# Kernel optimization log

Measured on AMD Instinct MI355X. Metric: run time of the kernel, lower is better.

Reference implementation:

```python
import jax, jax.numpy as jnp
import numpy as np

DIM = 64; N_LAYER = 2; B = 2048; M = 64
N_ENT = 100000; N_REL = 200
TEMP = 0.2; KGE_W = 1e-6
MIN_N = 1e-15; BND = 1e-5


def _norm(x):
    return jnp.sqrt(jnp.clip((x * x).sum(-1, keepdims=True), MIN_N))


def _l2(x):
    # F.normalize(p=2): x / max(||x||, 1e-12)
    return x / jnp.maximum(jnp.sqrt((x * x).sum(-1, keepdims=True)), 1e-12)


def _artanh(x):
    return jnp.arctanh(jnp.clip(x, -1.0 + BND, 1.0 - BND))


def expmap0(u):
    n = _norm(u)
    return jnp.tanh(n) * u / n


def logmap0(x):
    n = _norm(x)
    return _artanh(n) * x / n


def mobius_add(x, y):
    x2 = (x * x).sum(-1, keepdims=True)
    y2 = (y * y).sum(-1, keepdims=True)
    xy = (x * y).sum(-1, keepdims=True)
    num = (1 + 2 * xy + y2) * x + (1 - x2) * y
    den = 1 + 2 * xy + x2 * y2
    return num / jnp.clip(den, MIN_N)


def expmap(u, p):
    lam = 2.0 / jnp.clip(1.0 - (p * p).sum(-1, keepdims=True), MIN_N)
    n = _norm(u)
    return mobius_add(p, jnp.tanh(lam * n / 2.0) * u / n)


def logmap(x, p):
    m = mobius_add(-p, x)
    n = _norm(m)
    lam = 2.0 / jnp.clip(1.0 - (p * p).sum(-1, keepdims=True), MIN_N)
    return (2.0 / lam) * _artanh(n) * m / n


def _ed_agg(h, path, t, att_w1, att_w2):
    # attention: Linear(2d,d,no bias) -> LeakyReLU(0)==ReLU -> Linear(d,1,no bias) -> Sigmoid
    x = jnp.concatenate([h, path], -1)                       # [B,M,2d]
    a = jax.nn.sigmoid(jax.nn.relu(x @ att_w1) @ att_w2)[..., 0]  # [B,M]
    w = jax.nn.softmax(a, axis=-1)
    return (w[..., None] * t).sum(1)                          # [B,d]


def _hyper_agg(h, path, t, curvature, a2_w1, a2_b1, a2_w2, a2_b2):
    h, path, t = _l2(h), _l2(path), _l2(t)
    hh = expmap0(h) * jnp.abs(curvature)
    ht = expmap(t, hh)
    hr = expmap(path, hh)
    tang = logmap0(jnp.concatenate([hh, hr], -1))            # [B,M,2d]
    a = jnp.tanh(jax.nn.relu(tang @ a2_w1 + a2_b1) @ a2_w2 + a2_b2)[..., 0]
    w = jax.nn.softmax(a, axis=-1)                            # [B,M]
    agg = w[..., None] * ht
    mean_pt = (w[..., None] * hh).sum(1, keepdims=True)       # [B,1,d]
    e = logmap(agg, mean_pt)
    return (w[..., None] * e).sum(1)                          # [B,d]


def _build(E, R, h_idx, r_idx, t_idx, init_emb, agg):
    embs = [init_emb]
    for i in range(N_LAYER):
        h = E[h_idx[0]]
        path = R[r_idx[0]]
        for k in range(1, i + 1):  # faithful to source: inner loop reuses index i
            h = h + E[h_idx[i]]
            path = path * R[r_idx[i]]
        embs.append(agg(h, path, E[t_idx[i]]))
    return jnp.stack(embs)  # [L+1, B, d]


def _mlcl(a_stack, b_stack):
    # vectorized over layer index i of MLCL_Loss(a[i], b[i], a_list, b_list)
    na, nb = _l2(a_stack), _l2(b_stack)                       # [L+1,B,d]
    d = na.shape[-1]
    pos = (na * nb).sum(-1)                                   # [L+1,B]
    ttl1 = jnp.einsum('lbd,md->lbm', na, nb.reshape(-1, d))
    ttl2 = jnp.einsum('lbd,md->lbm', nb, na.reshape(-1, d))
    ep = jnp.exp(pos / TEMP)
    l1 = -jnp.log(ep / jnp.exp(ttl1 / TEMP).sum(-1)).sum()
    l2 = -jnp.log(ep / jnp.exp(ttl2 / TEMP).sum(-1)).sum()
    return KGE_W * (l1 + l2)


def _cat_rev(stack):
    # e = stack[0]; for i in 1..L: e = cat(stack[i], e) -> [L, L-1, ..., 0]
    return jnp.concatenate([stack[i] for i in range(stack.shape[0] - 1, -1, -1)], -1)


def setup_inputs() -> dict:
    key = jax.random.key(0)
    ks = jax.random.split(key, 24)
    def ent_idx(k):
        return jax.random.randint(k, (N_LAYER, B, M), 0, N_ENT, dtype=jnp.int32)
    def rel_idx(k):
        return jax.random.randint(k, (N_LAYER, B, M), 0, N_REL, dtype=jnp.int32)
    inp = {
        'items': jax.random.randint(ks[0], (B,), 0, N_ENT, dtype=jnp.int32),
        'ucf_h': ent_idx(ks[1]), 'ucf_r': rel_idx(ks[2]), 'ucf_t': ent_idx(ks[3]),
        'ikg_h': ent_idx(ks[4]), 'ikg_r': rel_idx(ks[5]), 'ikg_t': ent_idx(ks[6]),
        'ukg_h': ent_idx(ks[7]), 'ukg_r': rel_idx(ks[8]), 'ukg_t': ent_idx(ks[9]),
        'icf_h': ent_idx(ks[10]), 'icf_r': rel_idx(ks[11]), 'icf_t': ent_idx(ks[12]),
        'ent_emb': jax.random.normal(ks[13], (N_ENT, DIM), jnp.float32) * 0.02,
        'rel_emb': jax.random.normal(ks[14], (N_REL, DIM), jnp.float32) * 0.02,
        'att_w1': jax.random.normal(ks[15], (2 * DIM, DIM), jnp.float32) * 0.05,
        'att_w2': jax.random.normal(ks[16], (DIM, 1), jnp.float32) * 0.05,
        'att2_w1': jax.random.normal(ks[17], (2 * DIM, DIM), jnp.float32) * 0.05,
        'att2_b1': jnp.zeros((DIM,), jnp.float32),
        'att2_w2': jax.random.normal(ks[18], (DIM, 1), jnp.float32) * 0.05,
        'att2_b2': jnp.zeros((1,), jnp.float32),
        'curvature': jnp.asarray(1.0, jnp.float32),
    }
    return inp


def reference(items, ucf_h, ucf_r, ucf_t, ikg_h, ikg_r, ikg_t,
              ukg_h, ukg_r, ukg_t, icf_h, icf_r, icf_t,
              ent_emb, rel_emb, att_w1, att_w2,
              att2_w1, att2_b1, att2_w2, att2_b2, curvature):
    ed = lambda h, p, t: _ed_agg(h, p, t, att_w1, att_w2)
    hy = lambda h, p, t: _hyper_agg(h, p, t, curvature, att2_w1, att2_b1, att2_w2, att2_b2)
    ucf = _build(ent_emb, rel_emb, ucf_h, ucf_r, ucf_t, ent_emb[ucf_h[0]].mean(1), ed)
    ikg = _build(ent_emb, rel_emb, ikg_h, ikg_r, ikg_t, ent_emb[items], ed)
    ukg = _build(ent_emb, rel_emb, ukg_h, ukg_r, ukg_t, ent_emb[ukg_h[0]].mean(1), hy)
    icf = _build(ent_emb, rel_emb, icf_h, icf_r, icf_t, ent_emb[icf_h[0]].mean(1), hy)
    kge_loss = _mlcl(ucf, ukg) + _mlcl(ikg, icf)
    e_u = jnp.concatenate([_cat_rev(ucf), _cat_rev(ukg)], -1)
    e_i = jnp.concatenate([_cat_rev(icf), _cat_rev(ikg)], -1)
    scores = jax.nn.sigmoid((e_i * e_u).sum(-1))
    return scores, kge_loss
```

## Files before the change

kernel.cpp:

```cpp
#include <hip/hip_runtime.h>
#include <hip/hip_bf16.h>
#include <cstdint>
#include <cstddef>

constexpr int NB = 2048;
constexpr int NM = 64;
constexpr int ND = 64;
constexpr int NBM = NB * NM;
constexpr int NROWS = 3 * NB;
constexpr int STACK = 3 * NB * ND;
constexpr int NZ = 8;

typedef __attribute__((ext_vector_type(8))) short short8;
typedef __attribute__((ext_vector_type(4))) float float4v;

__device__ __forceinline__ float wsum(float v) {
#pragma unroll
  for (int o = 32; o > 0; o >>= 1) v += __shfl_xor(v, o, 64);
  return v;
}

__device__ __forceinline__ float wmax(float v) {
#pragma unroll
  for (int o = 32; o > 0; o >>= 1) v = fmaxf(v, __shfl_xor(v, o, 64));
  return v;
}

__device__ __forceinline__ float rcpf(float x) { return __builtin_amdgcn_rcpf(x); }
__device__ __forceinline__ float sqf(float x) { return __builtin_amdgcn_sqrtf(x); }

__device__ __forceinline__ float fast_tanh(float x) {
  float t = __expf(2.f * x);
  return (t - 1.f) * rcpf(t + 1.f);
}

__device__ __forceinline__ float artanh_clip(float x) {
  x = fminf(fmaxf(x, -1.f + 1e-5f), 1.f - 1e-5f);
  return 0.5f * __logf((1.f + x) * rcpf(1.f - x));
}

__device__ __forceinline__ ushort f2bf(float f) {
  return (ushort)((__float_as_uint(f) + 0x8000u) >> 16);
}
__device__ __forceinline__ float bf2f(ushort u) {
  return __uint_as_float((uint)u << 16);
}
__device__ __forceinline__ uint pack_bf2(float h, float p) {
  uint hu = __float_as_uint(h) + 0x8000u;
  uint pu = __float_as_uint(p) + 0x8000u;
  return __builtin_amdgcn_perm(pu, hu, 0x07060302);
}
__device__ __forceinline__ float hp_lo(uint v) { return __uint_as_float(v << 16); }
__device__ __forceinline__ float hp_hi(uint v) { return __uint_as_float(v & 0xFFFF0000u); }

__device__ __forceinline__ float readlane_f(float v, int l) {
  return __int_as_float(__builtin_amdgcn_readlane(__float_as_int(v), l));
}

__device__ __forceinline__ void write_row_norm(
    float v, float* __restrict__ frow, ushort* __restrict__ nrow, int lane) {
  float nv = wsum(v * v);
  float r = rcpf(fmaxf(sqf(nv), 1e-12f));
  frow[lane] = v;
  nrow[lane] = f2bf(v * r);
}

__global__ __launch_bounds__(64) void prep_kernel(
    const float* __restrict__ E, const int* __restrict__ items,
    const float* __restrict__ w1_ed, const float* __restrict__ w1_hy,
    float* __restrict__ s_ikg, ushort* __restrict__ nbf_ikg,
    ushort* __restrict__ w1p_ed, ushort* __restrict__ w1p_hy) {
  int blk = blockIdx.x, lane = threadIdx.x;
  if (blk < NB) {
    float v = E[(size_t)items[blk] * ND + lane];
    write_row_norm(v, s_ikg + (size_t)blk * ND, nbf_ikg + (size_t)blk * ND, lane);
  } else {
    int e = (blk - NB) * 64 + lane;
    const float* w1 = (e < 8192) ? w1_ed : w1_hy;
    ushort* out = (e < 8192) ? w1p_ed : w1p_hy;
    e &= 8191;
    int j = e & 7, ln = (e >> 3) & 63, nt = (e >> 9) & 3, kt = e >> 11;
    int n = nt * 16 + (ln & 15), k = kt * 32 + ((ln >> 4) << 3) + j;
    out[e] = f2bf(w1[k * 64 + n]);
  }
}

constexpr int OFF_H = 0;
constexpr int OFF_P = 4608;
constexpr int OFF_T = 9728;
constexpr int XS = 152;
constexpr int REGA_SZ = 14336;

__global__ __launch_bounds__(256) void agg_all_kernel(
    const float* __restrict__ E, const float* __restrict__ R,
    const int* __restrict__ h0, const int* __restrict__ r0, const int* __restrict__ t0,
    const int* __restrict__ h1, const int* __restrict__ r1, const int* __restrict__ t1,
    const int* __restrict__ h2, const int* __restrict__ r2, const int* __restrict__ t2,
    const int* __restrict__ h3, const int* __restrict__ r3, const int* __restrict__ t3,
    const ushort* __restrict__ w1p_ed, const float* __restrict__ w2_ed,
    const ushort* __restrict__ w1p_hy, const float* __restrict__ b1,
    const float* __restrict__ w2_hy, const float* __restrict__ b2,
    const float* __restrict__ curv,
    float* __restrict__ stacks, ushort* __restrict__ nbf) {
  __shared__ __align__(16) ushort regA[REGA_SZ];
  __shared__ float a_s[64];
  __shared__ float part[4][64];
  __shared__ float minit[4][64];

  const int b = blockIdx.x;
  const int fam = blockIdx.y;
  const int tid = threadIdx.x;
  const int wave = tid >> 6, lane = tid & 63;
  const int m0 = __builtin_amdgcn_readfirstlane(wave) * 16;
  const int colq = lane & 15, quad = lane >> 4;
  const size_t L = (size_t)NB * ND;

  const int* h_idx = (fam == 0) ? h0 : (fam == 1) ? h1 : (fam == 2) ? h2 : h3;
  const int* r_idx = (fam == 0) ? r0 : (fam == 1) ? r1 : (fam == 2) ? r2 : r3;
  const int* t_idx = (fam == 0) ? t0 : (fam == 1) ? t1 : (fam == 2) ? t2 : t3;
  float* sb = stacks + (size_t)fam * STACK;
  ushort* nb = nbf + (size_t)fam * STACK;

  uint hp[16];

  if (fam < 2) {
    const int do_init = (fam == 0);
    for (int layer = 0; layer < 2; ++layer) {
      float tv[16];
      if (layer == 0) {
        float macc = 0.f;
#pragma unroll
        for (int mi = 0; mi < 16; ++mi) {
          const int m = m0 + mi;
          float hd = E[(size_t)h_idx[b * NM + m] * ND + lane];
          float pd = R[(size_t)r_idx[b * NM + m] * ND + lane];
          macc += hd;
          uint pk = pack_bf2(hd, pd);
          hp[mi] = pk;
          regA[m * XS + lane] = (ushort)pk;
          regA[m * XS + 64 + lane] = (ushort)(pk >> 16);
        }
        if (do_init) minit[wave][lane] = macc;
      } else {
#pragma unroll
        for (int mi = 0; mi < 16; ++mi) {
          const int m = m0 + mi;
          float hd = hp_lo(hp[mi]) + E[(size_t)h_idx[NBM + b * NM + m] * ND + lane];
          float pd = hp_hi(hp[mi]) * R[(size_t)r_idx[NBM + b * NM + m] * ND + lane];
          uint pk = pack_bf2(hd, pd);
          hp[mi] = pk;
          regA[m * XS + lane] = (ushort)pk;
          regA[m * XS + 64 + lane] = (ushort)(pk >> 16);
        }
      }
#pragma unroll
      for (int mi = 0; mi < 16; ++mi)
        tv[mi] = E[(size_t)t_idx[(size_t)layer * NBM + b * NM + m0 + mi] * ND + lane];

      {
        short8 afr[4];
#pragma unroll
        for (int kt = 0; kt < 4; ++kt)
          afr[kt] = *(const short8*)&regA[(m0 + colq) * XS + kt * 32 + quad * 8];
        float w2v[4];
#pragma unroll
        for (int nt = 0; nt < 4; ++nt) w2v[nt] = w2_ed[nt * 16 + colq];
        float cc[4][4];
#pragma unroll
        for (int nt = 0; nt < 4; ++nt) {
          float4v c = {0.f, 0.f, 0.f, 0.f};
#pragma unroll
          for (int kt = 0; kt < 4; ++kt) {
            short8 bfr = *(const short8*)&w1p_ed[(((kt << 2) | nt) * 64 + lane) * 8];
            c = __builtin_amdgcn_mfma_f32_16x16x32_bf16(afr[kt], bfr, c, 0, 0, 0);
          }
#pragma unroll
          for (int i = 0; i < 4; ++i) cc[nt][i] = c[i];
        }
        float sred[4];
#pragma unroll
        for (int i = 0; i < 4; ++i)
          sred[i] = fmaxf(cc[0][i], 0.f) * w2v[0] + fmaxf(cc[1][i], 0.f) * w2v[1] +
                    fmaxf(cc[2][i], 0.f) * w2v[2] + fmaxf(cc[3][i], 0.f) * w2v[3];
#pragma unroll
        for (int o = 8; o > 0; o >>= 1) {
#pragma unroll
          for (int i = 0; i < 4; ++i) sred[i] += __shfl_xor(sred[i], o, 64);
        }
        if (colq == 0) {
#pragma unroll
          for (int i = 0; i < 4; ++i)
            a_s[m0 + quad * 4 + i] = 1.f / (1.f + __expf(-sred[i]));
        }
      }
      __syncthreads();

      float wl;
      {
        float v = a_s[lane];
        float mx = wmax(v);
        float e = __expf(v - mx);
        wl = e / wsum(e);
      }
      if (layer == 0 && do_init && wave == 0) {
        float v = (minit[0][lane] + minit[1][lane] + minit[2][lane] + minit[3][lane]) * (1.f / 64.f);
        write_row_norm(v, sb + (size_t)b * ND, nb + (size_t)b * ND, lane);
      }

      float o = 0.f;
#pragma unroll
      for (int mi = 0; mi < 16; ++mi)
        o = fmaf(readlane_f(wl, m0 + mi), tv[mi], o);
      part[wave][lane] = o;
      __syncthreads();
      if (wave == 0) {
        float v = part[0][lane] + part[1][lane] + part[2][lane] + part[3][lane];
        write_row_norm(v, sb + (layer + 1) * L + (size_t)b * ND,
                       nb + (layer + 1) * L + (size_t)b * ND, lane);
      }
    }
  } else {
    const float cabs = fabsf(*curv);
    const int j = colq;
    const int srcl = ((j >> 2) << 4) + j;

    for (int layer = 0; layer < 2; ++layer) {
      if (layer == 0) {
        float macc = 0.f;
#pragma unroll
        for (int mi = 0; mi < 16; ++mi) {
          const int m = m0 + mi;
          float hd = E[(size_t)h_idx[b * NM + m] * ND + lane];
          float pd = R[(size_t)r_idx[b * NM + m] * ND + lane];
          float td = E[(size_t)t_idx[b * NM + m] * ND + lane];
          macc += hd;
          uint pk = pack_bf2(hd, pd);
          hp[mi] = pk;
          regA[OFF_H + m * 72 + lane] = (ushort)pk;
          regA[OFF_P + m * 72 + lane] = (ushort)(pk >> 16);
          regA[OFF_T + m * 72 + lane] = f2bf(td);
        }
        part[wave][lane] = macc;
      } else {
#pragma unroll
        for (int mi = 0; mi < 16; ++mi) {
          const int m = m0 + mi;
          float hd = hp_lo(hp[mi]) + E[(size_t)h_idx[NBM + b * NM + m] * ND + lane];
          float pd = hp_hi(hp[mi]) * R[(size_t)r_idx[NBM + b * NM + m] * ND + lane];
          float td = E[(size_t)t_idx[(size_t)NBM + b * NM + m] * ND + lane];
          uint pk = pack_bf2(hd, pd);
          hp[mi] = pk;
          regA[OFF_H + m * 72 + lane] = (ushort)pk;
          regA[OFF_P + m * 72 + lane] = (ushort)(pk >> 16);
          regA[OFF_T + m * 72 + lane] = f2bf(td);
        }
      }

      float sh, sp, st, sht, shp;
      {
        const int fr = m0 + colq;
        const ushort* pH = &regA[OFF_H + fr * 72 + quad * 8];
        const ushort* pP = &regA[OFF_P + fr * 72 + quad * 8];
        const ushort* pT = &regA[OFF_T + fr * 72 + quad * 8];
        short8 hh0 = *(const short8*)pH, hh1 = *(const short8*)(pH + 32);
        short8 pp0 = *(const short8*)pP, pp1 = *(const short8*)(pP + 32);
        short8 tt0 = *(const short8*)pT, tt1 = *(const short8*)(pT + 32);
        const int dr = colq & 3;
#define DIAG_DOT(OUTV, A0, A1, B0, B1)                                      \
        {                                                                    \
          float4v c = {0.f, 0.f, 0.f, 0.f};                                  \
          c = __builtin_amdgcn_mfma_f32_16x16x32_bf16(A0, B0, c, 0, 0, 0);   \
          c = __builtin_amdgcn_mfma_f32_16x16x32_bf16(A1, B1, c, 0, 0, 0);   \
          float dv = (dr & 2) ? ((dr & 1) ? c[3] : c[2])                     \
                              : ((dr & 1) ? c[1] : c[0]);                    \
          OUTV = __shfl(dv, srcl, 64);                                       \
        }
        DIAG_DOT(sh, hh0, hh1, hh0, hh1)
        DIAG_DOT(sp, pp0, pp1, pp0, pp1)
        DIAG_DOT(st, tt0, tt1, tt0, tt1)
        DIAG_DOT(sht, hh0, hh1, tt0, tt1)
        DIAG_DOT(shp, hh0, hh1, pp0, pp1)
#undef DIAG_DOT
      }

      float g_ch, g_e1, g_e2, g_gh, g_q1, g_q2, g_hts2;
      {
        float rih = rcpf(fmaxf(sqf(sh), 1e-12f));
        float rip = rcpf(fmaxf(sqf(sp), 1e-12f));
        float rit = rcpf(fmaxf(sqf(st), 1e-12f));
        float nh = sqf(fmaxf(sh * rih * rih, 1e-15f));
        float ch = fast_tanh(nh) * rcpf(nh) * rih * cabs;
        float p2 = ch * ch * sh;
        float lam = 2.f * rcpf(fmaxf(1.f - p2, 1e-15f));
        float ntn = sqf(fmaxf(st * rit * rit, 1e-15f));
        float ct = fast_tanh(0.5f * lam * ntn) * rcpf(ntn) * rit;
        float y2 = ct * ct * st, xy = ch * ct * sht;
        float At = 1.f + 2.f * xy + y2, Bt = 1.f - p2;
        float rdt = rcpf(fmaxf(1.f + 2.f * xy + p2 * y2, 1e-15f));
        g_e1 = At * ch * rdt;
        g_e2 = Bt * ct * rdt;
        g_hts2 = g_e1 * g_e1 * sh + 2.f * g_e1 * g_e2 * sht + g_e2 * g_e2 * st;
        float npn = sqf(fmaxf(sp * rip * rip, 1e-15f));
        float cp = fast_tanh(0.5f * lam * npn) * rcpf(npn) * rip;
        float z2 = cp * cp * sp, xz = ch * cp * shp;
        float Ar = 1.f + 2.f * xz + z2;
        float rdr = rcpf(fmaxf(1.f + 2.f * xz + p2 * z2, 1e-15f));
        float f1 = Ar * ch * rdr, f2 = Bt * cp * rdr;
        float hr2 = f1 * f1 * sh + 2.f * f1 * f2 * shp + f2 * f2 * sp;
        float n128 = sqf(fmaxf(p2 + hr2, 1e-15f));
        float fq = artanh_clip(n128) * rcpf(n128);
        g_ch = ch;
        g_gh = fq * ch;
        g_q1 = fq * f1;
        g_q2 = fq * f2;
      }

      __syncthreads();
      if (layer == 0 && wave == 0) {
        float v = (part[0][lane] + part[1][lane] + part[2][lane] + part[3][lane]) * (1.f / 64.f);
        write_row_norm(v, sb + (size_t)b * ND, nb + (size_t)b * ND, lane);
      }

#pragma unroll
      for (int mi = 0; mi < 16; ++mi) {
        const int m = m0 + mi;
        float hvf = hp_lo(hp[mi]);
        float pvf = hp_hi(hp[mi]);
        float tvf = bf2f(regA[OFF_T + m * 72 + lane]);
        float ghm = readlane_f(g_gh, mi);
        float q1m = readlane_f(g_q1, mi);
        float q2m = readlane_f(g_q2, mi);
        float e1m = readlane_f(g_e1, mi);
        float e2m = readlane_f(g_e2, mi);
        regA[m * XS + lane] = f2bf(ghm * hvf);
        regA[m * XS + 64 + lane] = f2bf(q1m * hvf + q2m * pvf);
        regA[OFF_T + m * 72 + lane] = f2bf(e1m * hvf + e2m * tvf);
      }

      {
        short8 afr[4];
#pragma unroll
        for (int kt = 0; kt < 4; ++kt)
          afr[kt] = *(const short8*)&regA[(m0 + colq) * XS + kt * 32 + quad * 8];
        float b1v[4], w2v[4];
#pragma unroll
        for (int nt = 0; nt < 4; ++nt) {
          b1v[nt] = b1[nt * 16 + colq];
          w2v[nt] = w2_hy[nt * 16 + colq];
        }
        float cc[4][4];
#pragma unroll
        for (int nt = 0; nt < 4; ++nt) {
          float4v c = {0.f, 0.f, 0.f, 0.f};
#pragma unroll
          for (int kt = 0; kt < 4; ++kt) {
            short8 bfr = *(const short8*)&w1p_hy[(((kt << 2) | nt) * 64 + lane) * 8];
            c = __builtin_amdgcn_mfma_f32_16x16x32_bf16(afr[kt], bfr, c, 0, 0, 0);
          }
#pragma unroll
          for (int i = 0; i < 4; ++i) cc[nt][i] = c[i];
        }
        float b2v = b2[0];
        float sred[4];
#pragma unroll
        for (int i = 0; i < 4; ++i)
          sred[i] = fmaxf(cc[0][i] + b1v[0], 0.f) * w2v[0] +
                    fmaxf(cc[1][i] + b1v[1], 0.f) * w2v[1] +
                    fmaxf(cc[2][i] + b1v[2], 0.f) * w2v[2] +
                    fmaxf(cc[3][i] + b1v[3], 0.f) * w2v[3];
#pragma unroll
        for (int o = 8; o > 0; o >>= 1) {
#pragma unroll
          for (int i = 0; i < 4; ++i) sred[i] += __shfl_xor(sred[i], o, 64);
        }
        if (colq == 0) {
#pragma unroll
          for (int i = 0; i < 4; ++i)
            a_s[m0 + quad * 4 + i] = fast_tanh(sred[i] + b2v);
        }
      }
      __syncthreads();

      float wl;
      {
        float v = a_s[lane];
        float mx = wmax(v);
        float e = __expf(v - mx);
        wl = e / wsum(e);
      }

      float mp = 0.f;
#pragma unroll
      for (int mi = 0; mi < 16; ++mi)
        mp = fmaf(readlane_f(wl, m0 + mi) * readlane_f(g_ch, mi), hp_lo(hp[mi]), mp);
      part[wave][lane] = mp;
      __syncthreads();

      float mv = part[0][lane] + part[1][lane] + part[2][lane] + part[3][lane];
      float p2m = wsum(mv * mv);

      float dpv;
      {
        const ushort* pA = &regA[OFF_T + (m0 + colq) * 72 + quad * 8];
        short8 a0 = *(const short8*)pA, a1 = *(const short8*)(pA + 32);
        short8 bm0, bm1;
#pragma unroll
        for (int jj = 0; jj < 8; ++jj) {
          bm0[jj] = (short)f2bf(__shfl(mv, quad * 8 + jj, 64));
          bm1[jj] = (short)f2bf(__shfl(mv, 32 + quad * 8 + jj, 64));
        }
        float4v c = {0.f, 0.f, 0.f, 0.f};
        c = __builtin_amdgcn_mfma_f32_16x16x32_bf16(a0, bm0, c, 0, 0, 0);
        c = __builtin_amdgcn_mfma_f32_16x16x32_bf16(a1, bm1, c, 0, 0, 0);
        const int dr = colq & 3;
        float dv = (dr & 2) ? ((dr & 1) ? c[3] : c[2]) : ((dr & 1) ? c[1] : c[0]);
        dpv = __shfl(dv, srcl, 64);
      }

      const float be = fmaxf(1.f - p2m, 1e-15f);
      float g1, g2;
      {
        float wm = __shfl(wl, m0 + j, 64);
        float y2 = wm * wm * g_hts2;
        float xy = -wm * dpv;
        float al = 1.f + 2.f * xy + y2;
        float rd = rcpf(fmaxf(1.f + 2.f * xy + p2m * y2, 1e-15f));
        float md2 = (al * al * p2m - 2.f * al * be * wm * dpv + be * be * y2) * rd * rd;
        float n = sqf(fmaxf(md2, 1e-15f));
        float sm = be * artanh_clip(n) * rcpf(n) * rd;
        g1 = wm * wm * sm * be;
        g2 = wm * sm * al;
      }
      float ovec = 0.f, cA = 0.f;
#pragma unroll
      for (int mi = 0; mi < 16; ++mi) {
        const int m = m0 + mi;
        float htf = bf2f(regA[OFF_T + m * 72 + lane]);
        ovec = fmaf(readlane_f(g1, mi), htf, ovec);
        cA += readlane_f(g2, mi);
      }
      part[wave][lane] = ovec - cA * mv;
      __syncthreads();
      if (wave == 0) {
        float v = part[0][lane] + part[1][lane] + part[2][lane] + part[3][lane];
        write_row_norm(v, sb + (layer + 1) * L + (size_t)b * ND,
                       nb + (layer + 1) * L + (size_t)b * ND, lane);
      }
    }
  }
}

__global__ __launch_bounds__(256) void pos_scores_kernel(
    const ushort* __restrict__ nbf, const float* __restrict__ stacks,
    float* __restrict__ pos, float* __restrict__ out) {
  int lane = threadIdx.x & 63;
  int wave = threadIdx.x >> 6;
  if (blockIdx.y < 2) {
    int row = blockIdx.x * 4 + wave;
    int sa = blockIdx.y;
    float a = bf2f(nbf[(size_t)sa * STACK + (size_t)row * ND + lane]);
    float c = bf2f(nbf[(size_t)(sa + 2) * STACK + (size_t)row * ND + lane]);
    float d = wsum(a * c);
    if (lane == 0) pos[sa * NROWS + row] = d;
  } else {
    int b = blockIdx.x * 4 + wave;
    if (b >= NB) return;
    float s = 0.f;
#pragma unroll
    for (int l = 0; l < 3; ++l) {
      size_t o = (size_t)l * NB * ND + (size_t)b * ND + lane;
      s += stacks[0 * (size_t)STACK + o] * stacks[3 * (size_t)STACK + o]
         + stacks[2 * (size_t)STACK + o] * stacks[1 * (size_t)STACK + o];
    }
    s = wsum(s);
    if (lane == 0) out[b] = 1.f / (1.f + __expf(-s));
  }
}

__global__ __launch_bounds__(256) void lse_mfma_kernel(
    const ushort* __restrict__ nbf, float* __restrict__ Spart) {
  __shared__ __align__(16) ushort ytile[2][64 * 72];
  const int tid = threadIdx.x;
  const int wave = tid >> 6, lane = tid & 63;
  const int pair = blockIdx.y;
  const int z = blockIdx.z;
  int xi = (pair & 2) ? ((pair & 1) ? 3 : 1) : ((pair & 1) ? 2 : 0);
  int yi = xi ^ 2;
  const ushort* X = nbf + (size_t)xi * STACK;
  const ushort* Y = nbf + (size_t)yi * STACK;
  const int r0 = blockIdx.x * 64 + wave * 16;
  const int row = lane & 15, quad = lane >> 4;

  short8 a0 = *(const short8*)&X[(size_t)(r0 + row) * 64 + quad * 8];
  short8 a1 = *(const short8*)&X[(size_t)(r0 + row) * 64 + 32 + quad * 8];

  const int srow = tid >> 2, schunk = tid & 3;
  constexpr int NT = (NROWS / NZ) / 64;
  const int c0 = z * (NROWS / NZ);
  const ushort* sg = &Y[(size_t)(c0 + srow) * 64 + schunk * 16];
  ushort* sl = &ytile[0][0] + srow * 72 + schunk * 16;

  {
    short8 s0 = *(const short8*)sg;
    short8 s1 = *(const short8*)(sg + 8);
    *(short8*)sl = s0;
    *(short8*)(sl + 8) = s1;
  }
  __syncthreads();

  float rsum[4] = {0.f, 0.f, 0.f, 0.f};
  for (int ct = 0; ct < NT; ++ct) {
    const int cur = ct & 1;
    short8 n0, n1;
    if (ct + 1 < NT) {
      const ushort* src = sg + (size_t)(ct + 1) * 64 * 64;
      n0 = *(const short8*)src;
      n1 = *(const short8*)(src + 8);
    }
#pragma unroll
    for (int nt = 0; nt < 4; ++nt) {
      const ushort* yr = &ytile[cur][(nt * 16 + row) * 72 + quad * 8];
      short8 b0 = *(const short8*)yr;
      short8 b1 = *(const short8*)(yr + 32);
      float4v c = {0.f, 0.f, 0.f, 0.f};
      c = __builtin_amdgcn_mfma_f32_16x16x32_bf16(a0, b0, c, 0, 0, 0);
      c = __builtin_amdgcn_mfma_f32_16x16x32_bf16(a1, b1, c, 0, 0, 0);
#pragma unroll
      for (int i = 0; i < 4; ++i) rsum[i] += __expf(c[i] * 5.f);
    }
    if (ct + 1 < NT) {
      ushort* dst = &ytile[0][0] + ((ct + 1) & 1) * (64 * 72) + srow * 72 + schunk * 16;
      *(short8*)dst = n0;
      *(short8*)(dst + 8) = n1;
      __syncthreads();
    }
  }
#pragma unroll
  for (int i = 0; i < 4; ++i) {
    float v = rsum[i];
    v += __shfl_xor(v, 1, 64);
    v += __shfl_xor(v, 2, 64);
    v += __shfl_xor(v, 4, 64);
    v += __shfl_xor(v, 8, 64);
    if (row == 0)
      Spart[((size_t)z * 4 + pair) * NROWS + r0 + quad * 4 + i] = v;
  }
}

__global__ __launch_bounds__(256) void loss_part_kernel(
    const float* __restrict__ Spart, const float* __restrict__ pos,
    double* __restrict__ lossp) {
  __shared__ double red[256];
  const int t = threadIdx.x, blk = blockIdx.x;
  double acc = 0.0;
#pragma unroll
  for (int r = 0; r < 2; ++r) {
    int i = blk * 512 + r * 256 + t;
    float s = 0.f;
#pragma unroll
    for (int zz = 0; zz < NZ; ++zz) s += Spart[i + zz * 4 * NROWS];
    acc += (double)__logf(s);
  }
  {
    int jj = blk * 256 + t;
    acc -= 10.0 * (double)pos[jj];
  }
  red[t] = acc;
  __syncthreads();
  for (int s = 128; s > 0; s >>= 1) {
    if (t < s) red[t] += red[t + s];
    __syncthreads();
  }
  if (t == 0) lossp[blk] = red[0];
}

__global__ __launch_bounds__(64) void loss_final_kernel(
    const double* __restrict__ lossp, float* __restrict__ out) {
  int lane = threadIdx.x;
  double v = (lane < 48) ? lossp[lane] : 0.0;
#pragma unroll
  for (int o = 32; o > 0; o >>= 1) v += __shfl_xor(v, o, 64);
  if (lane == 0) out[NB] = (float)(1e-6 * v);
}

extern "C" void kernel_launch(void* const* d_in, const int* in_sizes, int n_in,
                              void* d_out, int out_size, void* d_ws, size_t ws_size,
                              hipStream_t stream) {
  const int* items = (const int*)d_in[0];
  const int* ucf_h = (const int*)d_in[1];
  const int* ucf_r = (const int*)d_in[2];
  const int* ucf_t = (const int*)d_in[3];
  const int* ikg_h = (const int*)d_in[4];
  const int* ikg_r = (const int*)d_in[5];
  const int* ikg_t = (const int*)d_in[6];
  const int* ukg_h = (const int*)d_in[7];
  const int* ukg_r = (const int*)d_in[8];
  const int* ukg_t = (const int*)d_in[9];
  const int* icf_h = (const int*)d_in[10];
  const int* icf_r = (const int*)d_in[11];
  const int* icf_t = (const int*)d_in[12];
  const float* E = (const float*)d_in[13];
  const float* R = (const float*)d_in[14];
  const float* att_w1 = (const float*)d_in[15];
  const float* att_w2 = (const float*)d_in[16];
  const float* a2_w1 = (const float*)d_in[17];
  const float* a2_b1 = (const float*)d_in[18];
  const float* a2_w2 = (const float*)d_in[19];
  const float* a2_b2 = (const float*)d_in[20];
  const float* curv = (const float*)d_in[21];
  float* outp = (float*)d_out;

  float* ws = (float*)d_ws;
  float* stacks = ws;
  float* Spart = stacks + 4 * (size_t)STACK;
  float* posarr = Spart + (size_t)NZ * 4 * NROWS;
  ushort* nbf = (ushort*)(posarr + 2 * (size_t)NROWS);
  ushort* w1p_ed = nbf + 4 * (size_t)STACK;
  ushort* w1p_hy = w1p_ed + 8192;
  double* lossp = (double*)(w1p_hy + 8192);

  float* ikg = stacks + 1 * (size_t)STACK;
  ushort* nbf_ikg = nbf + 1 * (size_t)STACK;

  prep_kernel<<<NB + 256, 64, 0, stream>>>(E, items, att_w1, a2_w1,
                                           ikg, nbf_ikg, w1p_ed, w1p_hy);

  agg_all_kernel<<<dim3(NB, 4), 256, 0, stream>>>(
      E, R,
      ucf_h, ucf_r, ucf_t, ikg_h, ikg_r, ikg_t,
      ukg_h, ukg_r, ukg_t, icf_h, icf_r, icf_t,
      w1p_ed, att_w2, w1p_hy, a2_b1, a2_w2, a2_b2, curv,
      stacks, nbf);

  pos_scores_kernel<<<dim3(NROWS / 4, 3), 256, 0, stream>>>(nbf, stacks, posarr, outp);
  lse_mfma_kernel<<<dim3(NROWS / 64, 4, NZ), 256, 0, stream>>>(nbf, Spart);

  loss_part_kernel<<<48, 256, 0, stream>>>(Spart, posarr, lossp);
  loss_final_kernel<<<1, 64, 0, stream>>>(lossp, outp);
}
```

Measured before the change: 343.1 us.

## Store normalized bf16 stacks in MFMA fragment order and drop LDS staging

Normalized bf16 embedding rows are now written in a 16-row tiled layout that matches the MFMA 16x16x32 operand fragment. The contrastive LSE kernel can then load B operands straight from global memory with contiguous 32-byte per-lane reads, with no LDS double buffering or barriers. The positive-score kernel is rewritten to read the same tiled layout, with one wave handling 16 rows. The cost is that every Y tile is re-read from global or L2 by each wave instead of being shared through LDS, and all producers and consumers must agree on the new layout.

```diff
diff --git a/kernel.cpp b/kernel.cpp
--- a/kernel.cpp
+++ b/kernel.cpp
@@ -58,11 +58,14 @@
 }
 
 __device__ __forceinline__ void write_row_norm(
-    float v, float* __restrict__ frow, ushort* __restrict__ nrow, int lane) {
+    float v, float* __restrict__ frow, ushort* __restrict__ nstack,
+    int r, int lane) {
   float nv = wsum(v * v);
-  float r = rcpf(fmaxf(sqf(nv), 1e-12f));
+  float rr = rcpf(fmaxf(sqf(nv), 1e-12f));
   frow[lane] = v;
-  nrow[lane] = f2bf(v * r);
+  int q = (lane >> 3) & 3, half = lane >> 5, j = lane & 7;
+  int fl = (r & 15) | (q << 4);
+  nstack[(size_t)(r >> 4) * 1024 + fl * 16 + half * 8 + j] = f2bf(v * rr);
 }
 
 __global__ __launch_bounds__(64) void prep_kernel(
@@ -73,7 +76,7 @@
   int blk = blockIdx.x, lane = threadIdx.x;
   if (blk < NB) {
     float v = E[(size_t)items[blk] * ND + lane];
-    write_row_norm(v, s_ikg + (size_t)blk * ND, nbf_ikg + (size_t)blk * ND, lane);
+    write_row_norm(v, s_ikg + (size_t)blk * ND, nbf_ikg, blk, lane);
   } else {
     int e = (blk - NB) * 64 + lane;
     const float* w1 = (e < 8192) ? w1_ed : w1_hy;
@@ -204,7 +207,7 @@
       }
       if (layer == 0 && do_init && wave == 0) {
         float v = (minit[0][lane] + minit[1][lane] + minit[2][lane] + minit[3][lane]) * (1.f / 64.f);
-        write_row_norm(v, sb + (size_t)b * ND, nb + (size_t)b * ND, lane);
+        write_row_norm(v, sb + (size_t)b * ND, nb, b, lane);
       }
 
       float o = 0.f;
@@ -216,7 +219,7 @@
       if (wave == 0) {
         float v = part[0][lane] + part[1][lane] + part[2][lane] + part[3][lane];
         write_row_norm(v, sb + (layer + 1) * L + (size_t)b * ND,
-                       nb + (layer + 1) * L + (size_t)b * ND, lane);
+                       nb, (layer + 1) * NB + b, lane);
       }
     }
   } else {
@@ -318,7 +321,7 @@
       __syncthreads();
       if (layer == 0 && wave == 0) {
         float v = (part[0][lane] + part[1][lane] + part[2][lane] + part[3][lane]) * (1.f / 64.f);
-        write_row_norm(v, sb + (size_t)b * ND, nb + (size_t)b * ND, lane);
+        write_row_norm(v, sb + (size_t)b * ND, nb, b, lane);
       }
 
 #pragma unroll
@@ -444,7 +447,7 @@
       if (wave == 0) {
         float v = part[0][lane] + part[1][lane] + part[2][lane] + part[3][lane];
         write_row_norm(v, sb + (layer + 1) * L + (size_t)b * ND,
-                       nb + (layer + 1) * L + (size_t)b * ND, lane);
+                       nb, (layer + 1) * NB + b, lane);
       }
     }
   }
@@ -456,12 +459,21 @@
   int lane = threadIdx.x & 63;
   int wave = threadIdx.x >> 6;
   if (blockIdx.y < 2) {
-    int row = blockIdx.x * 4 + wave;
+    if (blockIdx.x >= 96) return;
+    int g = blockIdx.x * 4 + wave;
     int sa = blockIdx.y;
-    float a = bf2f(nbf[(size_t)sa * STACK + (size_t)row * ND + lane]);
-    float c = bf2f(nbf[(size_t)(sa + 2) * STACK + (size_t)row * ND + lane]);
-    float d = wsum(a * c);
-    if (lane == 0) pos[sa * NROWS + row] = d;
+    const ushort* X = nbf + (size_t)sa * STACK + (size_t)g * 1024 + lane * 16;
+    const ushort* Yp = nbf + (size_t)(sa + 2) * STACK + (size_t)g * 1024 + lane * 16;
+    short8 x0 = *(const short8*)X, x1 = *(const short8*)(X + 8);
+    short8 y0 = *(const short8*)Yp, y1 = *(const short8*)(Yp + 8);
+    float d = 0.f;
+#pragma unroll
+    for (int jj = 0; jj < 8; ++jj)
+      d += bf2f((ushort)x0[jj]) * bf2f((ushort)y0[jj]) +
+           bf2f((ushort)x1[jj]) * bf2f((ushort)y1[jj]);
+    d += __shfl_xor(d, 16, 64);
+    d += __shfl_xor(d, 32, 64);
+    if (lane < 16) pos[sa * NROWS + g * 16 + lane] = d;
   } else {
     int b = blockIdx.x * 4 + wave;
     if (b >= NB) return;
@@ -479,7 +491,6 @@
 
 __global__ __launch_bounds__(256) void lse_mfma_kernel(
     const ushort* __restrict__ nbf, float* __restrict__ Spart) {
-  __shared__ __align__(16) ushort ytile[2][64 * 72];
   const int tid = threadIdx.x;
   const int wave = tid >> 6, lane = tid & 63;
   const int pair = blockIdx.y;
@@ -489,51 +500,24 @@
   const ushort* X = nbf + (size_t)xi * STACK;
   const ushort* Y = nbf + (size_t)yi * STACK;
   const int r0 = blockIdx.x * 64 + wave * 16;
+  const int g = r0 >> 4;
   const int row = lane & 15, quad = lane >> 4;
-
-  short8 a0 = *(const short8*)&X[(size_t)(r0 + row) * 64 + quad * 8];
-  short8 a1 = *(const short8*)&X[(size_t)(r0 + row) * 64 + 32 + quad * 8];
-
-  const int srow = tid >> 2, schunk = tid & 3;
-  constexpr int NT = (NROWS / NZ) / 64;
-  const int c0 = z * (NROWS / NZ);
-  const ushort* sg = &Y[(size_t)(c0 + srow) * 64 + schunk * 16];
-  ushort* sl = &ytile[0][0] + srow * 72 + schunk * 16;
-
-  {
-    short8 s0 = *(const short8*)sg;
-    short8 s1 = *(const short8*)(sg + 8);
-    *(short8*)sl = s0;
-    *(short8*)(sl + 8) = s1;
-  }
-  __syncthreads();
+  (void)quad;
+
+  short8 a0 = *(const short8*)&X[(size_t)g * 1024 + lane * 16];
+  short8 a1 = *(const short8*)&X[(size_t)g * 1024 + lane * 16 + 8];
 
   float rsum[4] = {0.f, 0.f, 0.f, 0.f};
-  for (int ct = 0; ct < NT; ++ct) {
-    const int cur = ct & 1;
-    short8 n0, n1;
-    if (ct + 1 < NT) {
-      const ushort* src = sg + (size_t)(ct + 1) * 64 * 64;
-      n0 = *(const short8*)src;
-      n1 = *(const short8*)(src + 8);
-    }
-#pragma unroll
-    for (int nt = 0; nt < 4; ++nt) {
-      const ushort* yr = &ytile[cur][(nt * 16 + row) * 72 + quad * 8];
-      short8 b0 = *(const short8*)yr;
-      short8 b1 = *(const short8*)(yr + 32);
-      float4v c = {0.f, 0.f, 0.f, 0.f};
-      c = __builtin_amdgcn_mfma_f32_16x16x32_bf16(a0, b0, c, 0, 0, 0);
-      c = __builtin_amdgcn_mfma_f32_16x16x32_bf16(a1, b1, c, 0, 0, 0);
-#pragma unroll
-      for (int i = 0; i < 4; ++i) rsum[i] += __expf(c[i] * 5.f);
-    }
-    if (ct + 1 < NT) {
-      ushort* dst = &ytile[0][0] + ((ct + 1) & 1) * (64 * 72) + srow * 72 + schunk * 16;
-      *(short8*)dst = n0;
-      *(short8*)(dst + 8) = n1;
-      __syncthreads();
-    }
+  const int cg0 = z * (NROWS / NZ / 16);
+  for (int ct = 0; ct < NROWS / NZ / 16; ++ct) {
+    const ushort* yp = &Y[(size_t)(cg0 + ct) * 1024 + lane * 16];
+    short8 b0 = *(const short8*)yp;
+    short8 b1 = *(const short8*)(yp + 8);
+    float4v c = {0.f, 0.f, 0.f, 0.f};
+    c = __builtin_amdgcn_mfma_f32_16x16x32_bf16(a0, b0, c, 0, 0, 0);
+    c = __builtin_amdgcn_mfma_f32_16x16x32_bf16(a1, b1, c, 0, 0, 0);
+#pragma unroll
+    for (int i = 0; i < 4; ++i) rsum[i] += __expf(c[i] * 5.f);
   }
 #pragma unroll
   for (int i = 0; i < 4; ++i) {
@@ -543,7 +527,7 @@
     v += __shfl_xor(v, 4, 64);
     v += __shfl_xor(v, 8, 64);
     if (row == 0)
-      Spart[((size_t)z * 4 + pair) * NROWS + r0 + quad * 4 + i] = v;
+      Spart[((size_t)z * 4 + pair) * NROWS + r0 + (lane >> 4) * 4 + i] = v;
   }
 }
 
@@ -632,7 +616,7 @@
       w1p_ed, att_w2, w1p_hy, a2_b1, a2_w2, a2_b2, curv,
       stacks, nbf);
 
-  pos_scores_kernel<<<dim3(NROWS / 4, 3), 256, 0, stream>>>(nbf, stacks, posarr, outp);
+  pos_scores_kernel<<<dim3(NB / 4, 3), 256, 0, stream>>>(nbf, stacks, posarr, outp);
   lse_mfma_kernel<<<dim3(NROWS / 64, 4, NZ), 256, 0, stream>>>(nbf, Spart);
 
   loss_part_kernel<<<48, 256, 0, stream>>>(Spart, posarr, lossp);
```

Result: slower. 385.3 us (+12.3%).
